# Kernel tuning notes

Hardware: AMD Instinct MI355X
Metric: run time of the kernel (lower is better)

## Reference

```python
import jax, jax.numpy as jnp
import numpy as np

N = 50000      # nodes
E = 800000     # edges
D_IN = 128
D_H = 128
D_OUT = 64


def setup_inputs() -> dict:
    key = jax.random.key(0)
    ks = jax.random.split(key, 10)
    x = jax.random.normal(ks[0], (N, D_IN), dtype=jnp.float32)
    edge_index = jax.random.randint(ks[1], (2, E), 0, N, dtype=jnp.int32)
    def glorot(k, fan_in, fan_out):
        s = jnp.sqrt(6.0 / (fan_in + fan_out)).astype(jnp.float32)
        return jax.random.uniform(k, (fan_in, fan_out), jnp.float32, -s, s)
    return {
        "x": x,
        "edge_index": edge_index,
        "W1": glorot(ks[2], D_IN, D_H), "b1": jnp.zeros((D_H,), jnp.float32),
        "W2": glorot(ks[3], D_H, D_H),  "b2": jnp.zeros((D_H,), jnp.float32),
        "W3": glorot(ks[4], D_H, D_H),  "b3": jnp.zeros((D_H,), jnp.float32),
        "Wfc": glorot(ks[5], D_H, D_OUT), "bfc": jnp.zeros((D_OUT,), jnp.float32),
    }


def gcn_conv(x, W, b, src, dst, n):
    h = x @ W                                   # [N, d_out]
    loop = jnp.arange(n, dtype=src.dtype)
    src_f = jnp.concatenate([src, loop])        # [E+N]
    dst_f = jnp.concatenate([dst, loop])
    deg = jax.ops.segment_sum(jnp.ones_like(dst_f, dtype=h.dtype), dst_f, num_segments=n)
    dinv = jnp.where(deg > 0, jax.lax.rsqrt(deg), 0.0)
    norm = dinv[src_f] * dinv[dst_f]            # [E+N]
    msgs = h[src_f] * norm[:, None]             # gather + scale
    out = jax.ops.segment_sum(msgs, dst_f, num_segments=n)  # scatter-add
    return out + b


def reference(x, edge_index, W1, b1, W2, b2, W3, b3, Wfc, bfc):
    src, dst = edge_index[0], edge_index[1]
    n = x.shape[0]
    h = x
    for W, b in ((W1, b1), (W2, b2), (W3, b3)):
        h = jax.nn.relu(gcn_conv(h, W, b, src, dst, n))
    # dropout is identity in eval mode
    return h @ Wfc + bfc
```

## Files before the change

kernel.cpp:

```cpp
#include <hip/hip_runtime.h>

#define NN 50000
#define EE 800000
#define DD 128
#define DOUTC 64
#define SLOTS 62
#define ROWB 128
#define BUCKET_BLKS 3125
#define ZERO_BLKS 1563

typedef unsigned int uint;
typedef unsigned short ushort;
typedef __attribute__((ext_vector_type(8))) short bf16x8;
typedef __attribute__((ext_vector_type(4))) float f32x4;

__device__ __forceinline__ float bf2f(uint b) { return __uint_as_float(b << 16); }
__device__ __forceinline__ ushort f2bf(float f) {
    uint u = __float_as_uint(f);
    u += 0x7fffu + ((u >> 16) & 1u);
    return (ushort)(u >> 16);
}

struct PreArgs {
    const float *w1, *w2, *w3, *wfc;
    ushort *wt1, *wt2, *wt3, *wtfc;
    char* colb;
};

__global__ __launch_bounds__(256) void k_pre(PreArgs a) {
    int b = blockIdx.x, t = threadIdx.x;
    if (b < ZERO_BLKS) {
        size_t i = ((size_t)b * 256 + t) * 16;
        if (i < (size_t)NN * ROWB) *(uint4*)(a.colb + i) = (uint4){0, 0, 0, 0};
    } else if (b < ZERO_BLKS + 192) {
        int b2 = b - ZERO_BLKS;
        const float* w = (b2 < 64) ? a.w1 : (b2 < 128) ? a.w2 : a.w3;
        ushort* wt = (b2 < 64) ? a.wt1 : (b2 < 128) ? a.wt2 : a.wt3;
        int idx = (b2 & 63) * 256 + t;
        int k = idx >> 7, n = idx & 127;
        wt[n * DD + k] = f2bf(w[idx]);
    } else {
        int idx = (b - ZERO_BLKS - 192) * 256 + t;
        int k = idx >> 6, n = idx & 63;
        a.wtfc[n * DD + k] = f2bf(a.wfc[idx]);
    }
}

__global__ __launch_bounds__(256) void k_bucket(
    const int* __restrict__ src, const int* __restrict__ dst,
    char* __restrict__ colb) {
    int e = blockIdx.x * 256 + threadIdx.x;
    int d = dst[e];
    int s = src[e];
    char* row = colb + ((size_t)d << 7);
    int p = atomicAdd((int*)row, 1);
    if (p < SLOTS) *(ushort*)(row + 4 + 2 * p) = (ushort)s;
}

__global__ __launch_bounds__(256) void k_mm1(
    const float* __restrict__ X, const ushort* __restrict__ WT,
    const char* __restrict__ colb, ushort* __restrict__ T) {
    const int wave = threadIdx.x >> 6;
    const int lane = threadIdx.x & 63;
    const int m0w = blockIdx.x * 64 + wave * 16;
    if (m0w >= NN) return;
    const int m = m0w + (lane & 15);
    const int quad = lane >> 4;
    f32x4 acc[8];
#pragma unroll
    for (int nt = 0; nt < 8; ++nt) acc[nt] = (f32x4){0.f, 0.f, 0.f, 0.f};
    const float* Hrow = X + (size_t)m * DD;
#pragma unroll
    for (int kk = 0; kk < 4; ++kk) {
        float4 a0 = *(const float4*)(Hrow + kk * 32 + quad * 8);
        float4 a1 = *(const float4*)(Hrow + kk * 32 + quad * 8 + 4);
        bf16x8 bfr;
        bfr[0] = (short)f2bf(a0.x); bfr[1] = (short)f2bf(a0.y);
        bfr[2] = (short)f2bf(a0.z); bfr[3] = (short)f2bf(a0.w);
        bfr[4] = (short)f2bf(a1.x); bfr[5] = (short)f2bf(a1.y);
        bfr[6] = (short)f2bf(a1.z); bfr[7] = (short)f2bf(a1.w);
#pragma unroll
        for (int nt = 0; nt < 8; ++nt) {
            bf16x8 afr = *(const bf16x8*)(WT + (size_t)(nt * 16 + (lane & 15)) * DD +
                                          kk * 32 + quad * 8);
            acc[nt] = __builtin_amdgcn_mfma_f32_16x16x32_bf16(afr, bfr, acc[nt], 0, 0, 0);
        }
    }
    int c = *(const int*)(colb + ((size_t)m << 7));
    float di = rsqrtf((float)(c + 1));
#pragma unroll
    for (int nt = 0; nt < 8; ++nt) {
        int n = nt * 16 + quad * 4;
        uint2 o;
        o.x = (uint)f2bf(acc[nt][0] * di) | ((uint)f2bf(acc[nt][1] * di) << 16);
        o.y = (uint)f2bf(acc[nt][2] * di) | ((uint)f2bf(acc[nt][3] * di) << 16);
        *(uint2*)(T + (size_t)m * DD + n) = o;
    }
}

__global__ __launch_bounds__(256) void k_mm(
    const ushort* __restrict__ H, const ushort* __restrict__ WT,
    const char* __restrict__ colb, ushort* __restrict__ T) {
    const int wave = threadIdx.x >> 6;
    const int lane = threadIdx.x & 63;
    const int m0w = blockIdx.x * 64 + wave * 16;
    if (m0w >= NN) return;
    const int m = m0w + (lane & 15);
    const int quad = lane >> 4;
    f32x4 acc[8];
#pragma unroll
    for (int nt = 0; nt < 8; ++nt) acc[nt] = (f32x4){0.f, 0.f, 0.f, 0.f};
    const ushort* Hrow = H + (size_t)m * DD;
#pragma unroll
    for (int kk = 0; kk < 4; ++kk) {
        bf16x8 bfr = *(const bf16x8*)(Hrow + kk * 32 + quad * 8);
#pragma unroll
        for (int nt = 0; nt < 8; ++nt) {
            bf16x8 afr = *(const bf16x8*)(WT + (size_t)(nt * 16 + (lane & 15)) * DD +
                                          kk * 32 + quad * 8);
            acc[nt] = __builtin_amdgcn_mfma_f32_16x16x32_bf16(afr, bfr, acc[nt], 0, 0, 0);
        }
    }
    int c = *(const int*)(colb + ((size_t)m << 7));
    float di = rsqrtf((float)(c + 1));
#pragma unroll
    for (int nt = 0; nt < 8; ++nt) {
        int n = nt * 16 + quad * 4;
        uint2 o;
        o.x = (uint)f2bf(acc[nt][0] * di) | ((uint)f2bf(acc[nt][1] * di) << 16);
        o.y = (uint)f2bf(acc[nt][2] * di) | ((uint)f2bf(acc[nt][3] * di) << 16);
        *(uint2*)(T + (size_t)m * DD + n) = o;
    }
}

__global__ __launch_bounds__(256) void k_agg(
    const ushort* __restrict__ T, const char* __restrict__ colb,
    const float* __restrict__ bias, ushort* __restrict__ A) {
    int node = blockIdx.x * 4 + (threadIdx.x >> 6);
    if (node >= NN) return;
    int lane = threadIdx.x & 63;
    const uint* Tv = (const uint*)T;
    size_t base = (size_t)node * 64;
    const char* row = colb + ((size_t)node << 7);
    int c = *(const int*)row;
    int end = c < SLOTS ? c : SLOTS;
    const ushort* bl = (const ushort*)(row + 4);
    uint w0 = Tv[base + lane];
    float ax = bf2f(w0 & 0xffffu), ay = bf2f(w0 >> 16);
    int e = 0;
    for (; e + 7 < end; e += 8) {
        uint vv[8];
#pragma unroll
        for (int q = 0; q < 8; ++q) vv[q] = Tv[(size_t)bl[e + q] * 64 + lane];
#pragma unroll
        for (int q = 0; q < 8; ++q) {
            ax += bf2f(vv[q] & 0xffffu);
            ay += bf2f(vv[q] >> 16);
        }
    }
    for (; e < end; ++e) {
        uint v = Tv[(size_t)bl[e] * 64 + lane];
        ax += bf2f(v & 0xffffu);
        ay += bf2f(v >> 16);
    }
    float di = rsqrtf((float)(c + 1));
    float2 bv = ((const float2*)bias)[lane];
    float o0 = fmaxf(fmaf(ax, di, bv.x), 0.f);
    float o1 = fmaxf(fmaf(ay, di, bv.y), 0.f);
    ((uint*)A)[base + lane] = (uint)f2bf(o0) | ((uint)f2bf(o1) << 16);
}

__global__ __launch_bounds__(256) void k_mm_final(
    const ushort* __restrict__ H, const ushort* __restrict__ WT,
    const float* __restrict__ bb, float* __restrict__ out) {
    const int wave = threadIdx.x >> 6;
    const int lane = threadIdx.x & 63;
    const int m0w = blockIdx.x * 64 + wave * 16;
    if (m0w >= NN) return;
    const int m = m0w + (lane & 15);
    const int quad = lane >> 4;
    f32x4 acc[4];
#pragma unroll
    for (int nt = 0; nt < 4; ++nt) acc[nt] = (f32x4){0.f, 0.f, 0.f, 0.f};
    const ushort* Hrow = H + (size_t)m * DD;
#pragma unroll
    for (int kk = 0; kk < 4; ++kk) {
        bf16x8 bfr = *(const bf16x8*)(Hrow + kk * 32 + quad * 8);
#pragma unroll
        for (int nt = 0; nt < 4; ++nt) {
            bf16x8 afr = *(const bf16x8*)(WT + (size_t)(nt * 16 + (lane & 15)) * DD +
                                          kk * 32 + quad * 8);
            acc[nt] = __builtin_amdgcn_mfma_f32_16x16x32_bf16(afr, bfr, acc[nt], 0, 0, 0);
        }
    }
#pragma unroll
    for (int nt = 0; nt < 4; ++nt) {
        int n = nt * 16 + quad * 4;
        float4 bvals = *(const float4*)(bb + n);
        float4 o = {acc[nt][0] + bvals.x, acc[nt][1] + bvals.y,
                    acc[nt][2] + bvals.z, acc[nt][3] + bvals.w};
        *(float4*)(out + (size_t)m * DOUTC + n) = o;
    }
}

extern "C" void kernel_launch(void* const* d_in, const int* in_sizes, int n_in,
                              void* d_out, int out_size, void* d_ws, size_t ws_size,
                              hipStream_t stream) {
    const float* x   = (const float*)d_in[0];
    const int*   ei  = (const int*)d_in[1];
    const float* W1  = (const float*)d_in[2];
    const float* b1  = (const float*)d_in[3];
    const float* W2  = (const float*)d_in[4];
    const float* b2  = (const float*)d_in[5];
    const float* W3  = (const float*)d_in[6];
    const float* b3  = (const float*)d_in[7];
    const float* Wfc = (const float*)d_in[8];
    const float* bfc = (const float*)d_in[9];

    char* ws = (char*)d_ws;
    size_t off = 0;
    auto take = [&](size_t bytes) {
        void* p = ws + off;
        off = (off + bytes + 255) & ~(size_t)255;
        return p;
    };
    char*   colb = (char*)take((size_t)NN * ROWB);
    ushort* T    = (ushort*)take((size_t)NN * DD * 2);
    ushort* A    = (ushort*)take((size_t)NN * DD * 2);
    ushort* WT1  = (ushort*)take((size_t)DD * DD * 2);
    ushort* WT2  = (ushort*)take((size_t)DD * DD * 2);
    ushort* WT3  = (ushort*)take((size_t)DD * DD * 2);
    ushort* WTfc = (ushort*)take((size_t)DOUTC * DD * 2);

    const int* src = ei;
    const int* dst = ei + EE;

    PreArgs pa;
    pa.w1 = W1; pa.w2 = W2; pa.w3 = W3; pa.wfc = Wfc;
    pa.wt1 = WT1; pa.wt2 = WT2; pa.wt3 = WT3; pa.wtfc = WTfc;
    pa.colb = colb;
    k_pre<<<ZERO_BLKS + 192 + 32, 256, 0, stream>>>(pa);

    const int mm_grid  = (NN + 63) / 64;
    const int agg_grid = (NN + 3) / 4;

    k_bucket<<<BUCKET_BLKS, 256, 0, stream>>>(src, dst, colb);
    k_mm1<<<mm_grid, 256, 0, stream>>>(x, WT1, colb, T);
    k_agg<<<agg_grid, 256, 0, stream>>>(T, colb, b1, A);
    k_mm<<<mm_grid, 256, 0, stream>>>(A, WT2, colb, T);
    k_agg<<<agg_grid, 256, 0, stream>>>(T, colb, b2, A);
    k_mm<<<mm_grid, 256, 0, stream>>>(A, WT3, colb, T);
    k_agg<<<agg_grid, 256, 0, stream>>>(T, colb, b3, A);
    k_mm_final<<<mm_grid, 256, 0, stream>>>(A, WTfc, bfc, (float*)d_out);
}
```

Measured before the change: 327.2 us.

## Split aggregation into feature-column passes and shard bucket counters four ways

Transformed features T are now stored as four column slabs of 32 features each. Aggregation runs four passes, one per slab, so each slab's gather working set (3.2 MB) is small enough to stay in cache. The bucket counters are split into four sub-buckets selected by edge index, which spreads atomic contention, and the per-node adjacency capacity rises to 128 slots. The cost is reading each adjacency list four times, one ushort per lane per gather instead of a packed pair, and a larger zero-fill and adjacency buffer.

New measurement: 545.1 us. +66.6%, slower.

```diff
diff --git a/kernel.cpp b/kernel.cpp
--- a/kernel.cpp
+++ b/kernel.cpp
@@ -4,10 +4,12 @@
 #define EE 800000
 #define DD 128
 #define DOUTC 64
-#define SLOTS 62
-#define ROWB 128
+#define SUBS 4
+#define SUBCAP 32
 #define BUCKET_BLKS 3125
-#define ZERO_BLKS 1563
+#define AGG_NB 6250
+#define CNT4_BYTES (SUBS * NN * 4)
+#define CNT4_ZBLKS 196
 
 typedef unsigned int uint;
 typedef unsigned short ushort;
@@ -24,23 +26,23 @@
 struct PreArgs {
     const float *w1, *w2, *w3, *wfc;
     ushort *wt1, *wt2, *wt3, *wtfc;
-    char* colb;
+    char* cnt4;
 };
 
 __global__ __launch_bounds__(256) void k_pre(PreArgs a) {
     int b = blockIdx.x, t = threadIdx.x;
-    if (b < ZERO_BLKS) {
+    if (b < CNT4_ZBLKS) {
         size_t i = ((size_t)b * 256 + t) * 16;
-        if (i < (size_t)NN * ROWB) *(uint4*)(a.colb + i) = (uint4){0, 0, 0, 0};
-    } else if (b < ZERO_BLKS + 192) {
-        int b2 = b - ZERO_BLKS;
+        if (i < (size_t)CNT4_BYTES) *(uint4*)(a.cnt4 + i) = (uint4){0, 0, 0, 0};
+    } else if (b < CNT4_ZBLKS + 192) {
+        int b2 = b - CNT4_ZBLKS;
         const float* w = (b2 < 64) ? a.w1 : (b2 < 128) ? a.w2 : a.w3;
         ushort* wt = (b2 < 64) ? a.wt1 : (b2 < 128) ? a.wt2 : a.wt3;
         int idx = (b2 & 63) * 256 + t;
         int k = idx >> 7, n = idx & 127;
         wt[n * DD + k] = f2bf(w[idx]);
     } else {
-        int idx = (b - ZERO_BLKS - 192) * 256 + t;
+        int idx = (b - CNT4_ZBLKS - 192) * 256 + t;
         int k = idx >> 6, n = idx & 63;
         a.wtfc[n * DD + k] = f2bf(a.wfc[idx]);
     }
@@ -48,18 +50,18 @@
 
 __global__ __launch_bounds__(256) void k_bucket(
     const int* __restrict__ src, const int* __restrict__ dst,
-    char* __restrict__ colb) {
+    int* __restrict__ cnt4, ushort* __restrict__ colb) {
     int e = blockIdx.x * 256 + threadIdx.x;
     int d = dst[e];
     int s = src[e];
-    char* row = colb + ((size_t)d << 7);
-    int p = atomicAdd((int*)row, 1);
-    if (p < SLOTS) *(ushort*)(row + 4 + 2 * p) = (ushort)s;
+    int sub = e & 3;
+    int p = atomicAdd(&cnt4[sub * NN + d], 1);
+    if (p < SUBCAP) colb[((size_t)d << 7) + sub * SUBCAP + p] = (ushort)s;
 }
 
 __global__ __launch_bounds__(256) void k_mm1(
     const float* __restrict__ X, const ushort* __restrict__ WT,
-    const char* __restrict__ colb, ushort* __restrict__ T) {
+    const int* __restrict__ cnt4, ushort* __restrict__ T) {
     const int wave = threadIdx.x >> 6;
     const int lane = threadIdx.x & 63;
     const int m0w = blockIdx.x * 64 + wave * 16;
@@ -86,7 +88,7 @@
             acc[nt] = __builtin_amdgcn_mfma_f32_16x16x32_bf16(afr, bfr, acc[nt], 0, 0, 0);
         }
     }
-    int c = *(const int*)(colb + ((size_t)m << 7));
+    int c = cnt4[m] + cnt4[NN + m] + cnt4[2 * NN + m] + cnt4[3 * NN + m];
     float di = rsqrtf((float)(c + 1));
 #pragma unroll
     for (int nt = 0; nt < 8; ++nt) {
@@ -94,13 +96,13 @@
         uint2 o;
         o.x = (uint)f2bf(acc[nt][0] * di) | ((uint)f2bf(acc[nt][1] * di) << 16);
         o.y = (uint)f2bf(acc[nt][2] * di) | ((uint)f2bf(acc[nt][3] * di) << 16);
-        *(uint2*)(T + (size_t)m * DD + n) = o;
+        *(uint2*)(T + ((size_t)(n >> 5) * NN * 32) + (size_t)m * 32 + (n & 31)) = o;
     }
 }
 
 __global__ __launch_bounds__(256) void k_mm(
     const ushort* __restrict__ H, const ushort* __restrict__ WT,
-    const char* __restrict__ colb, ushort* __restrict__ T) {
+    const int* __restrict__ cnt4, ushort* __restrict__ T) {
     const int wave = threadIdx.x >> 6;
     const int lane = threadIdx.x & 63;
     const int m0w = blockIdx.x * 64 + wave * 16;
@@ -121,7 +123,7 @@
             acc[nt] = __builtin_amdgcn_mfma_f32_16x16x32_bf16(afr, bfr, acc[nt], 0, 0, 0);
         }
     }
-    int c = *(const int*)(colb + ((size_t)m << 7));
+    int c = cnt4[m] + cnt4[NN + m] + cnt4[2 * NN + m] + cnt4[3 * NN + m];
     float di = rsqrtf((float)(c + 1));
 #pragma unroll
     for (int nt = 0; nt < 8; ++nt) {
@@ -129,45 +131,42 @@
         uint2 o;
         o.x = (uint)f2bf(acc[nt][0] * di) | ((uint)f2bf(acc[nt][1] * di) << 16);
         o.y = (uint)f2bf(acc[nt][2] * di) | ((uint)f2bf(acc[nt][3] * di) << 16);
-        *(uint2*)(T + (size_t)m * DD + n) = o;
+        *(uint2*)(T + ((size_t)(n >> 5) * NN * 32) + (size_t)m * 32 + (n & 31)) = o;
     }
 }
 
 __global__ __launch_bounds__(256) void k_agg(
-    const ushort* __restrict__ T, const char* __restrict__ colb,
-    const float* __restrict__ bias, ushort* __restrict__ A) {
-    int node = blockIdx.x * 4 + (threadIdx.x >> 6);
-    if (node >= NN) return;
-    int lane = threadIdx.x & 63;
-    const uint* Tv = (const uint*)T;
-    size_t base = (size_t)node * 64;
-    const char* row = colb + ((size_t)node << 7);
-    int c = *(const int*)row;
-    int end = c < SLOTS ? c : SLOTS;
-    const ushort* bl = (const ushort*)(row + 4);
-    uint w0 = Tv[base + lane];
-    float ax = bf2f(w0 & 0xffffu), ay = bf2f(w0 >> 16);
-    int e = 0;
-    for (; e + 7 < end; e += 8) {
-        uint vv[8];
-#pragma unroll
-        for (int q = 0; q < 8; ++q) vv[q] = Tv[(size_t)bl[e + q] * 64 + lane];
-#pragma unroll
-        for (int q = 0; q < 8; ++q) {
-            ax += bf2f(vv[q] & 0xffffu);
-            ay += bf2f(vv[q] >> 16);
-        }
-    }
-    for (; e < end; ++e) {
-        uint v = Tv[(size_t)bl[e] * 64 + lane];
-        ax += bf2f(v & 0xffffu);
-        ay += bf2f(v >> 16);
-    }
-    float di = rsqrtf((float)(c + 1));
-    float2 bv = ((const float2*)bias)[lane];
-    float o0 = fmaxf(fmaf(ax, di, bv.x), 0.f);
-    float o1 = fmaxf(fmaf(ay, di, bv.y), 0.f);
-    ((uint*)A)[base + lane] = (uint)f2bf(o0) | ((uint)f2bf(o1) << 16);
+    const ushort* __restrict__ Tc, const int* __restrict__ cnt4,
+    const ushort* __restrict__ colb, const float* __restrict__ bias,
+    ushort* __restrict__ A) {
+    int b = blockIdx.x;
+    int pass = b / AGG_NB;
+    int node = (b % AGG_NB) * 8 + (threadIdx.x >> 5);
+    int f = threadIdx.x & 31;
+    const ushort* Tp = Tc + (size_t)pass * NN * 32;
+    float ax = bf2f((uint)Tp[(size_t)node * 32 + f]);
+    int c0 = cnt4[node], c1 = cnt4[NN + node];
+    int c2 = cnt4[2 * NN + node], c3 = cnt4[3 * NN + node];
+    const ushort* row = colb + ((size_t)node << 7);
+#pragma unroll
+    for (int s = 0; s < 4; ++s) {
+        int cs = (s == 0) ? c0 : (s == 1) ? c1 : (s == 2) ? c2 : c3;
+        if (cs > SUBCAP) cs = SUBCAP;
+        const ushort* bl = row + s * SUBCAP;
+        int e = 0;
+        for (; e + 3 < cs; e += 4) {
+            int j0 = bl[e], j1 = bl[e + 1], j2 = bl[e + 2], j3 = bl[e + 3];
+            float v0 = bf2f((uint)Tp[(size_t)j0 * 32 + f]);
+            float v1 = bf2f((uint)Tp[(size_t)j1 * 32 + f]);
+            float v2 = bf2f((uint)Tp[(size_t)j2 * 32 + f]);
+            float v3 = bf2f((uint)Tp[(size_t)j3 * 32 + f]);
+            ax += (v0 + v1) + (v2 + v3);
+        }
+        for (; e < cs; ++e) ax += bf2f((uint)Tp[(size_t)bl[e] * 32 + f]);
+    }
+    float di = rsqrtf((float)(c0 + c1 + c2 + c3 + 1));
+    float o = fmaxf(fmaf(ax, di, bias[pass * 32 + f]), 0.f);
+    A[(size_t)node * DD + pass * 32 + f] = f2bf(o);
 }
 
 __global__ __launch_bounds__(256) void k_mm_final(
@@ -224,7 +223,8 @@
         off = (off + bytes + 255) & ~(size_t)255;
         return p;
     };
-    char*   colb = (char*)take((size_t)NN * ROWB);
+    int*    cnt4 = (int*)take(CNT4_BYTES);
+    ushort* colb = (ushort*)take((size_t)NN * 256);
     ushort* T    = (ushort*)take((size_t)NN * DD * 2);
     ushort* A    = (ushort*)take((size_t)NN * DD * 2);
     ushort* WT1  = (ushort*)take((size_t)DD * DD * 2);
@@ -238,18 +238,18 @@
     PreArgs pa;
     pa.w1 = W1; pa.w2 = W2; pa.w3 = W3; pa.wfc = Wfc;
     pa.wt1 = WT1; pa.wt2 = WT2; pa.wt3 = WT3; pa.wtfc = WTfc;
-    pa.colb = colb;
-    k_pre<<<ZERO_BLKS + 192 + 32, 256, 0, stream>>>(pa);
+    pa.cnt4 = (char*)cnt4;
+    k_pre<<<CNT4_ZBLKS + 192 + 32, 256, 0, stream>>>(pa);
 
     const int mm_grid  = (NN + 63) / 64;
-    const int agg_grid = (NN + 3) / 4;
-
-    k_bucket<<<BUCKET_BLKS, 256, 0, stream>>>(src, dst, colb);
-    k_mm1<<<mm_grid, 256, 0, stream>>>(x, WT1, colb, T);
-    k_agg<<<agg_grid, 256, 0, stream>>>(T, colb, b1, A);
-    k_mm<<<mm_grid, 256, 0, stream>>>(A, WT2, colb, T);
-    k_agg<<<agg_grid, 256, 0, stream>>>(T, colb, b2, A);
-    k_mm<<<mm_grid, 256, 0, stream>>>(A, WT3, colb, T);
-    k_agg<<<agg_grid, 256, 0, stream>>>(T, colb, b3, A);
+    const int agg_grid = 4 * AGG_NB;
+
+    k_bucket<<<BUCKET_BLKS, 256, 0, stream>>>(src, dst, cnt4, colb);
+    k_mm1<<<mm_grid, 256, 0, stream>>>(x, WT1, cnt4, T);
+    k_agg<<<agg_grid, 256, 0, stream>>>(T, cnt4, colb, b1, A);
+    k_mm<<<mm_grid, 256, 0, stream>>>(A, WT2, cnt4, T);
+    k_agg<<<agg_grid, 256, 0, stream>>>(T, cnt4, colb, b2, A);
+    k_mm<<<mm_grid, 256, 0, stream>>>(A, WT3, cnt4, T);
+    k_agg<<<agg_grid, 256, 0, stream>>>(T, cnt4, colb, b3, A);
     k_mm_final<<<mm_grid, 256, 0, stream>>>(A, WTfc, bfc, (float*)d_out);
 }
```

## Fuse neighbor aggregation with the following dense matmul per node tile

Applied to the files above, without the earlier changes.

Merges each aggregation kernel with the next layer's matmul (or the final FC) into one kernel. Each wave gathers and aggregates 16 nodes sequentially into shared memory, then runs MFMA on that tile directly, ping-ponging between two T buffers. This removes the intermediate activation write/read and three kernel launches. In exchange, parallelism per node drops from one wave per node to one wave per 16 nodes processed serially, which may reduce memory-latency hiding in the gather phase.

After: 376.9 us. +15.2%, slower.

```diff
diff --git a/kernel.cpp b/kernel.cpp
--- a/kernel.cpp
+++ b/kernel.cpp
@@ -98,108 +98,91 @@
     }
 }
 
-__global__ __launch_bounds__(256) void k_mm(
-    const ushort* __restrict__ H, const ushort* __restrict__ WT,
-    const char* __restrict__ colb, ushort* __restrict__ T) {
+template <bool FINAL>
+__global__ __launch_bounds__(256) void k_aggmm(
+    const ushort* __restrict__ T, const char* __restrict__ colb,
+    const float* __restrict__ bias, const ushort* __restrict__ WT,
+    const float* __restrict__ bfc, void* __restrict__ out_) {
+    __shared__ ushort As[4][16][136];
+    __shared__ float sdi[4][16];
     const int wave = threadIdx.x >> 6;
     const int lane = threadIdx.x & 63;
-    const int m0w = blockIdx.x * 64 + wave * 16;
-    if (m0w >= NN) return;
-    const int m = m0w + (lane & 15);
+    const uint* Tv = (const uint*)T;
+
+    for (int t = 0; t < 16; ++t) {
+        int node = blockIdx.x * 64 + wave * 16 + t;
+        float ax = 0.f, ay = 0.f, di = 1.f;
+        if (node < NN) {
+            const char* row = colb + ((size_t)node << 7);
+            int c = *(const int*)row;
+            int end = c < SLOTS ? c : SLOTS;
+            const ushort* bl = (const ushort*)(row + 4);
+            uint w0 = Tv[(size_t)node * 64 + lane];
+            ax = bf2f(w0 & 0xffffu); ay = bf2f(w0 >> 16);
+            int e = 0;
+            for (; e + 7 < end; e += 8) {
+                uint vv[8];
+#pragma unroll
+                for (int q = 0; q < 8; ++q) vv[q] = Tv[(size_t)bl[e + q] * 64 + lane];
+#pragma unroll
+                for (int q = 0; q < 8; ++q) {
+                    ax += bf2f(vv[q] & 0xffffu);
+                    ay += bf2f(vv[q] >> 16);
+                }
+            }
+            for (; e < end; ++e) {
+                uint v = Tv[(size_t)bl[e] * 64 + lane];
+                ax += bf2f(v & 0xffffu);
+                ay += bf2f(v >> 16);
+            }
+            di = rsqrtf((float)(c + 1));
+            float2 bv = ((const float2*)bias)[lane];
+            ax = fmaxf(fmaf(ax, di, bv.x), 0.f);
+            ay = fmaxf(fmaf(ay, di, bv.y), 0.f);
+        }
+        *(uint*)&As[wave][t][2 * lane] = (uint)f2bf(ax) | ((uint)f2bf(ay) << 16);
+        if (lane == 0) sdi[wave][t] = di;
+    }
+
+    const int mloc = lane & 15;
     const int quad = lane >> 4;
+    const int m = blockIdx.x * 64 + wave * 16 + mloc;
+    const int NT = FINAL ? 4 : 8;
     f32x4 acc[8];
 #pragma unroll
     for (int nt = 0; nt < 8; ++nt) acc[nt] = (f32x4){0.f, 0.f, 0.f, 0.f};
-    const ushort* Hrow = H + (size_t)m * DD;
 #pragma unroll
     for (int kk = 0; kk < 4; ++kk) {
-        bf16x8 bfr = *(const bf16x8*)(Hrow + kk * 32 + quad * 8);
-#pragma unroll
-        for (int nt = 0; nt < 8; ++nt) {
-            bf16x8 afr = *(const bf16x8*)(WT + (size_t)(nt * 16 + (lane & 15)) * DD +
+        bf16x8 bfr = *(const bf16x8*)&As[wave][mloc][kk * 32 + quad * 8];
+#pragma unroll
+        for (int nt = 0; nt < NT; ++nt) {
+            bf16x8 afr = *(const bf16x8*)(WT + (size_t)(nt * 16 + mloc) * DD +
                                           kk * 32 + quad * 8);
             acc[nt] = __builtin_amdgcn_mfma_f32_16x16x32_bf16(afr, bfr, acc[nt], 0, 0, 0);
         }
     }
-    int c = *(const int*)(colb + ((size_t)m << 7));
-    float di = rsqrtf((float)(c + 1));
-#pragma unroll
-    for (int nt = 0; nt < 8; ++nt) {
-        int n = nt * 16 + quad * 4;
-        uint2 o;
-        o.x = (uint)f2bf(acc[nt][0] * di) | ((uint)f2bf(acc[nt][1] * di) << 16);
-        o.y = (uint)f2bf(acc[nt][2] * di) | ((uint)f2bf(acc[nt][3] * di) << 16);
-        *(uint2*)(T + (size_t)m * DD + n) = o;
-    }
-}
-
-__global__ __launch_bounds__(256) void k_agg(
-    const ushort* __restrict__ T, const char* __restrict__ colb,
-    const float* __restrict__ bias, ushort* __restrict__ A) {
-    int node = blockIdx.x * 4 + (threadIdx.x >> 6);
-    if (node >= NN) return;
-    int lane = threadIdx.x & 63;
-    const uint* Tv = (const uint*)T;
-    size_t base = (size_t)node * 64;
-    const char* row = colb + ((size_t)node << 7);
-    int c = *(const int*)row;
-    int end = c < SLOTS ? c : SLOTS;
-    const ushort* bl = (const ushort*)(row + 4);
-    uint w0 = Tv[base + lane];
-    float ax = bf2f(w0 & 0xffffu), ay = bf2f(w0 >> 16);
-    int e = 0;
-    for (; e + 7 < end; e += 8) {
-        uint vv[8];
-#pragma unroll
-        for (int q = 0; q < 8; ++q) vv[q] = Tv[(size_t)bl[e + q] * 64 + lane];
-#pragma unroll
-        for (int q = 0; q < 8; ++q) {
-            ax += bf2f(vv[q] & 0xffffu);
-            ay += bf2f(vv[q] >> 16);
-        }
-    }
-    for (; e < end; ++e) {
-        uint v = Tv[(size_t)bl[e] * 64 + lane];
-        ax += bf2f(v & 0xffffu);
-        ay += bf2f(v >> 16);
-    }
-    float di = rsqrtf((float)(c + 1));
-    float2 bv = ((const float2*)bias)[lane];
-    float o0 = fmaxf(fmaf(ax, di, bv.x), 0.f);
-    float o1 = fmaxf(fmaf(ay, di, bv.y), 0.f);
-    ((uint*)A)[base + lane] = (uint)f2bf(o0) | ((uint)f2bf(o1) << 16);
-}
-
-__global__ __launch_bounds__(256) void k_mm_final(
-    const ushort* __restrict__ H, const ushort* __restrict__ WT,
-    const float* __restrict__ bb, float* __restrict__ out) {
-    const int wave = threadIdx.x >> 6;
-    const int lane = threadIdx.x & 63;
-    const int m0w = blockIdx.x * 64 + wave * 16;
-    if (m0w >= NN) return;
-    const int m = m0w + (lane & 15);
-    const int quad = lane >> 4;
-    f32x4 acc[4];
-#pragma unroll
-    for (int nt = 0; nt < 4; ++nt) acc[nt] = (f32x4){0.f, 0.f, 0.f, 0.f};
-    const ushort* Hrow = H + (size_t)m * DD;
-#pragma unroll
-    for (int kk = 0; kk < 4; ++kk) {
-        bf16x8 bfr = *(const bf16x8*)(Hrow + kk * 32 + quad * 8);
+    if (m >= NN) return;
+    if (FINAL) {
+        float* out = (float*)out_;
 #pragma unroll
         for (int nt = 0; nt < 4; ++nt) {
-            bf16x8 afr = *(const bf16x8*)(WT + (size_t)(nt * 16 + (lane & 15)) * DD +
-                                          kk * 32 + quad * 8);
-            acc[nt] = __builtin_amdgcn_mfma_f32_16x16x32_bf16(afr, bfr, acc[nt], 0, 0, 0);
-        }
-    }
-#pragma unroll
-    for (int nt = 0; nt < 4; ++nt) {
-        int n = nt * 16 + quad * 4;
-        float4 bvals = *(const float4*)(bb + n);
-        float4 o = {acc[nt][0] + bvals.x, acc[nt][1] + bvals.y,
-                    acc[nt][2] + bvals.z, acc[nt][3] + bvals.w};
-        *(float4*)(out + (size_t)m * DOUTC + n) = o;
+            int n = nt * 16 + quad * 4;
+            float4 bvals = *(const float4*)(bfc + n);
+            float4 o = {acc[nt][0] + bvals.x, acc[nt][1] + bvals.y,
+                        acc[nt][2] + bvals.z, acc[nt][3] + bvals.w};
+            *(float4*)(out + (size_t)m * DOUTC + n) = o;
+        }
+    } else {
+        ushort* T2 = (ushort*)out_;
+        float di2 = sdi[wave][mloc];
+#pragma unroll
+        for (int nt = 0; nt < 8; ++nt) {
+            int n = nt * 16 + quad * 4;
+            uint2 o;
+            o.x = (uint)f2bf(acc[nt][0] * di2) | ((uint)f2bf(acc[nt][1] * di2) << 16);
+            o.y = (uint)f2bf(acc[nt][2] * di2) | ((uint)f2bf(acc[nt][3] * di2) << 16);
+            *(uint2*)(T2 + (size_t)m * DD + n) = o;
+        }
     }
 }
 
@@ -226,7 +209,7 @@
     };
     char*   colb = (char*)take((size_t)NN * ROWB);
     ushort* T    = (ushort*)take((size_t)NN * DD * 2);
-    ushort* A    = (ushort*)take((size_t)NN * DD * 2);
+    ushort* T2   = (ushort*)take((size_t)NN * DD * 2);
     ushort* WT1  = (ushort*)take((size_t)DD * DD * 2);
     ushort* WT2  = (ushort*)take((size_t)DD * DD * 2);
     ushort* WT3  = (ushort*)take((size_t)DD * DD * 2);
@@ -241,15 +224,11 @@
     pa.colb = colb;
     k_pre<<<ZERO_BLKS + 192 + 32, 256, 0, stream>>>(pa);
 
-    const int mm_grid  = (NN + 63) / 64;
-    const int agg_grid = (NN + 3) / 4;
+    const int mm_grid = (NN + 63) / 64;
 
     k_bucket<<<BUCKET_BLKS, 256, 0, stream>>>(src, dst, colb);
     k_mm1<<<mm_grid, 256, 0, stream>>>(x, WT1, colb, T);
-    k_agg<<<agg_grid, 256, 0, stream>>>(T, colb, b1, A);
-    k_mm<<<mm_grid, 256, 0, stream>>>(A, WT2, colb, T);
-    k_agg<<<agg_grid, 256, 0, stream>>>(T, colb, b2, A);
-    k_mm<<<mm_grid, 256, 0, stream>>>(A, WT3, colb, T);
-    k_agg<<<agg_grid, 256, 0, stream>>>(T, colb, b3, A);
-    k_mm_final<<<mm_grid, 256, 0, stream>>>(A, WTfc, bfc, (float*)d_out);
-}
+    k_aggmm<false><<<mm_grid, 256, 0, stream>>>(T, colb, b1, WT2, nullptr, T2);
+    k_aggmm<false><<<mm_grid, 256, 0, stream>>>(T2, colb, b2, WT3, nullptr, T);
+    k_aggmm<true><<<mm_grid, 256, 0, stream>>>(T, colb, b3, WTfc, bfc, d_out);
+}
```
